# Kernel tuning notes

Hardware: AMD Instinct MI355X
Metric: run time of the kernel (lower is better)

Reference implementation:

```python
import jax, jax.numpy as jnp
import numpy as np

GAMMA = 1.0
MAX_SIMILARITY = 1.0


def setup_inputs() -> dict:
    key = jax.random.key(0)
    k1, k2 = jax.random.split(key)
    B, Ns, D = 128, 512, 256
    d_vectors = jax.random.normal(k1, (B, Ns, D), dtype=jnp.float32)
    # Normalized similarity matrix (MinMaxScaler output lies in [0, 1])
    S = jax.random.uniform(k2, (Ns, Ns), dtype=jnp.float32)
    return {"d_vectors": d_vectors, "S": S}


def reference(d_vectors, S):
    B, Ns, D = d_vectors.shape
    eye = jnp.eye(Ns, dtype=d_vectors.dtype)

    # Pairwise squared distances: ||di||^2 + ||dj||^2 - 2 di.dj  -> [B, Ns, Ns]
    n2 = jnp.sum(d_vectors * d_vectors, axis=-1)  # [B, Ns]
    sq = n2[:, :, None] + n2[:, None, :] - 2.0 * jnp.einsum("bid,bjd->bij", d_vectors, d_vectors)
    sq = jnp.maximum(sq, 0.0) * (1.0 - eye)  # exact zero on the diagonal

    # Safe sqrt (subgradient 0 at zero distance, matching torch.norm)
    dist = jnp.where(sq > 0, jnp.sqrt(jnp.where(sq > 0, sq, 1.0)), 0.0)
    Kd = jnp.exp(-GAMMA * dist)  # Gaussian-kernel Gram matrix [B, Ns, Ns]

    # Norm-ratio loss
    W = (S > 0).astype(d_vectors.dtype)  # [Ns, Ns]
    denom = jnp.linalg.norm(W - eye)  # Frobenius norm, scalar
    Kd_tilde = Kd * (1.0 - eye)  # zero diagonal
    S_tilde = S - MAX_SIMILARITY * eye
    diff = W * (Kd_tilde - S_tilde)  # broadcast over batch
    numer = jnp.sqrt(jnp.sum(diff * diff, axis=(1, 2)))  # [B]
    losses = 2.0 * numer / denom
    return jnp.sum(losses)
```

## Files before the change

kernel.cpp:

```cpp
#include <hip/hip_runtime.h>
#include <hip/hip_bf16.h>

typedef __bf16 bf16_t;
typedef __bf16 bf16x4 __attribute__((ext_vector_type(4)));
typedef __bf16 bf16x8 __attribute__((ext_vector_type(8)));
typedef float f32x4 __attribute__((ext_vector_type(4)));
typedef float f32x16 __attribute__((ext_vector_type(16)));
typedef long i64x2 __attribute__((ext_vector_type(2)));
typedef int i32x4 __attribute__((ext_vector_type(4)));

#define BATCH 128
#define NS 512
#define DIM 256
#define NTB 20
#define LDSP 272
#define CST 68

__global__ __launch_bounds__(256) void prep_st_kernel(const float* __restrict__ dv,
                                                      const float* __restrict__ S,
                                                      unsigned char* __restrict__ f8,
                                                      float* __restrict__ n2g,
                                                      float* __restrict__ St,
                                                      float* __restrict__ dpartial) {
    const int bidx = blockIdx.x;
    const int t = threadIdx.x;
    if (bidx < 256) {
        const int bi = bidx >> 4, bj = bidx & 15;
        const int c  = t & 31, r0 = t >> 5;
        __shared__ float tileS[32][33];
        __shared__ float red[4];
        float dacc = 0.0f;
#pragma unroll
        for (int k = 0; k < 4; ++k) {
            const int r  = r0 + k * 8;
            const int gi = bi * 32 + r, gj = bj * 32 + c;
            const float s = S[(size_t)gi * NS + gj];
            tileS[r][c] = s;
            const float w = (s > 0.0f) ? 1.0f : 0.0f;
            const float e = (gi == gj) ? 1.0f : 0.0f;
            const float d = w - e;
            dacc += d * d;
        }
        __syncthreads();
#pragma unroll
        for (int k = 0; k < 4; ++k) {
            const int r = r0 + k * 8;
            St[(size_t)(bj * 32 + r) * NS + bi * 32 + c] = tileS[c][r];
        }
        const int lane = t & 63, wave = t >> 6;
#pragma unroll
        for (int off = 32; off >= 1; off >>= 1) dacc += __shfl_down(dacc, off, 64);
        if (lane == 0) red[wave] = dacc;
        __syncthreads();
        if (t == 0) dpartial[bidx] = red[0] + red[1] + red[2] + red[3];
    } else {
        const int wid  = ((bidx - 256) << 2) | (t >> 6);
        const int lane = t & 63;
#pragma unroll
        for (int it = 0; it < 8; ++it) {
            const int row = wid + it * 8192;
            const f32x4 v = *reinterpret_cast<const f32x4*>(dv + (size_t)row * DIM + lane * 4);
            float pn = v[0]*v[0] + v[1]*v[1] + v[2]*v[2] + v[3]*v[3];
#pragma unroll
            for (int off = 32; off >= 1; off >>= 1) pn += __shfl_xor(pn, off, 64);
            int w0 = __builtin_amdgcn_cvt_pk_fp8_f32(v[0], v[1], 0, false);
            w0     = __builtin_amdgcn_cvt_pk_fp8_f32(v[2], v[3], w0, true);
            *reinterpret_cast<int*>(f8 + (size_t)row * DIM + lane * 4) = w0;
            if (lane == 0) n2g[row] = pn;
        }
    }
}

__global__ __launch_bounds__(512, 6) void gram_pair_kernel(const unsigned char* __restrict__ f8,
                                                           const float* __restrict__ n2g,
                                                           const float* __restrict__ S,
                                                           const float* __restrict__ St,
                                                           float* __restrict__ partial) {
    const int bid  = blockIdx.x;
    const int work = (bid & 7) * 320 + (bid >> 3);
    const int b    = work / NTB;
    const int r20  = work - b * NTB;
    int ti, tjc;
    if (r20 < 8)       { ti = 0; tjc = r20; }
    else if (r20 < 14) { ti = 1; tjc = r20 - 6; }
    else if (r20 < 18) { ti = 2; tjc = r20 - 10; }
    else               { ti = 3; tjc = r20 - 12; }
    const bool single = ((tjc >> 1) == ti);
    const int t    = threadIdx.x;
    const int wave = t >> 6, lane = t & 63;
    const int wr   = wave >> 1, wc = wave & 1;
    const int col  = lane & 31, kh = lane >> 5;

    __shared__ __attribute__((aligned(16))) char smem[192 * LDSP];
    __shared__ float n2s[192];
    __shared__ float red[8];
    char*  sP = smem;
    float* sC = reinterpret_cast<float*>(smem);

    {
        const unsigned char* srcA = f8 + ((size_t)b * NS + (size_t)ti * 128) * DIM;
#pragma unroll
        for (int it = 0; it < 4; ++it) {
            const i32x4 v = *reinterpret_cast<const i32x4*>(srcA + it * 8192 + t * 16);
            *reinterpret_cast<i32x4*>(&sP[(it * 32 + (t >> 4)) * LDSP + (t & 15) * 16]) = v;
        }
        const unsigned char* srcB = f8 + ((size_t)b * NS + (size_t)tjc * 64) * DIM;
#pragma unroll
        for (int it = 0; it < 2; ++it) {
            const i32x4 v = *reinterpret_cast<const i32x4*>(srcB + it * 8192 + t * 16);
            *reinterpret_cast<i32x4*>(&sP[(128 + it * 32 + (t >> 4)) * LDSP + (t & 15) * 16]) = v;
        }
        if (t < 128)      n2s[t] = n2g[(size_t)b * NS + (size_t)ti * 128 + t];
        else if (t < 192) n2s[t] = n2g[(size_t)b * NS + (size_t)tjc * 64 + (t - 128)];
    }
    __syncthreads();

    const char* aP = &sP[(wr * 32 + col) * LDSP + kh * 16];
    const char* bP = &sP[(128 + wc * 32 + col) * LDSP + kh * 16];
    f32x16 acc = (f32x16)(0.0f);
    __builtin_amdgcn_s_setprio(1);
#pragma unroll
    for (int u = 0; u < 8; ++u) {
        const i64x2 Av = *reinterpret_cast<const i64x2*>(aP + u * 32);
        const i64x2 Bv = *reinterpret_cast<const i64x2*>(bP + u * 32);
        acc = __builtin_amdgcn_mfma_f32_32x32x16_fp8_fp8(Av[0], Bv[0], acc, 0, 0, 0);
        acc = __builtin_amdgcn_mfma_f32_32x32x16_fp8_fp8(Av[1], Bv[1], acc, 0, 0, 0);
    }
    __builtin_amdgcn_s_setprio(0);
    __syncthreads();

    {
        const int lj = wc * 32 + col;
        const float n2j = n2s[128 + lj];
#pragma unroll
        for (int h4 = 0; h4 < 4; ++h4) {
#pragma unroll
            for (int e = 0; e < 4; ++e) {
                const int li = wr * 32 + h4 * 8 + kh * 4 + e;
                const float c = acc[h4 * 4 + e];
                const float sq = fmaxf(n2s[li] + n2j - 2.0f * c, 0.0f);
                sC[li * CST + lj] = __expf(-__builtin_amdgcn_sqrtf(sq));
            }
        }
    }
    __syncthreads();

    float local = 0.0f;
    {
        const int rg = t >> 4;
        const int ln = t & 15;
        f32x4 s1a[4], s2a[4];
#pragma unroll
        for (int p = 0; p < 4; ++p) {
            const int li = p * 32 + rg;
            const int gi = ti * 128 + li;
            const int cb = tjc * 64 + ln * 4;
            s1a[p] = *reinterpret_cast<const f32x4*>(S + (size_t)gi * NS + cb);
            s2a[p] = single ? (f32x4)(0.0f)
                            : *reinterpret_cast<const f32x4*>(St + (size_t)gi * NS + cb);
        }
#pragma unroll
        for (int p = 0; p < 4; ++p) {
            const int li = p * 32 + rg;
            const int gi = ti * 128 + li;
            const f32x4 kdv = *reinterpret_cast<const f32x4*>(&sC[li * CST + ln * 4]);
#pragma unroll
            for (int e = 0; e < 4; ++e) {
                const int gj = tjc * 64 + ln * 4 + e;
                const float kd = kdv[e];
                const float s1 = s1a[p][e];
                if (single) {
                    float d = (gi == gj) ? (1.0f - s1) : (kd - s1);
                    d *= (s1 > 0.0f) ? 1.0f : 0.0f;
                    local += d * d;
                } else {
                    const float s2 = s2a[p][e];
                    const float d1 = (s1 > 0.0f) ? (kd - s1) : 0.0f;
                    const float d2 = (s2 > 0.0f) ? (kd - s2) : 0.0f;
                    local += d1 * d1 + d2 * d2;
                }
            }
        }
    }

#pragma unroll
    for (int off = 32; off >= 1; off >>= 1) local += __shfl_down(local, off, 64);
    if (lane == 0) red[wave] = local;
    __syncthreads();
    if (t == 0) {
        float s = 0.0f;
#pragma unroll
        for (int w = 0; w < 8; ++w) s += red[w];
        partial[(size_t)b * NTB + r20] = s;
    }
}


__global__ __launch_bounds__(256) void norms_kernel(const float* __restrict__ dv,
                                                    float* __restrict__ n2) {
    const int row  = blockIdx.x * 4 + (threadIdx.x >> 6);
    const int lane = threadIdx.x & 63;
    const float4 v = *reinterpret_cast<const float4*>(dv + (size_t)row * DIM + lane * 4);
    float s = v.x * v.x + v.y * v.y + v.z * v.z + v.w * v.w;
#pragma unroll
    for (int off = 32; off >= 1; off >>= 1) s += __shfl_down(s, off, 64);
    if (lane == 0) n2[row] = s;
}

__global__ __launch_bounds__(256) void denom_kernel(const float* __restrict__ Smat,
                                                    float* __restrict__ dpartial) {
    const int t = threadIdx.x;
    const int lane = t & 63, wave = t >> 6;
    __shared__ float sred[4];
    float acc = 0.0f;
    const int base = blockIdx.x * 512;
#pragma unroll
    for (int r = 0; r < 2; ++r) {
        const int v4 = base + r * 256 + t;
        const float4 s4 = reinterpret_cast<const float4*>(Smat)[v4];
        const int idx0 = v4 * 4;
        const int i = idx0 >> 9;
#pragma unroll
        for (int c = 0; c < 4; ++c) {
            const float s = (&s4.x)[c];
            const int j = (idx0 + c) & (NS - 1);
            const float w = (s > 0.0f) ? 1.0f : 0.0f;
            const float e = (i == j) ? 1.0f : 0.0f;
            const float d = w - e;
            acc += d * d;
        }
    }
#pragma unroll
    for (int off = 32; off >= 1; off >>= 1) acc += __shfl_down(acc, off, 64);
    if (lane == 0) sred[wave] = acc;
    __syncthreads();
    if (t == 0) dpartial[blockIdx.x] = sred[0] + sred[1] + sred[2] + sred[3];
}

#define FLDSK 40
__global__ __launch_bounds__(256) void gram_f32_kernel(const float* __restrict__ dv,
                                                       const float* __restrict__ Smat,
                                                       const float* __restrict__ n2,
                                                       float* __restrict__ partial) {
    const int tile = blockIdx.x;
    const int b    = blockIdx.y;
    const int ti   = tile >> 2, tj = tile & 3;
    const int t    = threadIdx.x;
    const int wave = t >> 6, lane = t & 63;
    const int wr   = wave >> 1, wc = wave & 1;

    __shared__ bf16_t sA[128 * FLDSK];
    __shared__ bf16_t sB[128 * FLDSK];
    __shared__ float red[4];

    const float* Abase = dv + ((size_t)b * NS + (size_t)ti * 128) * DIM;
    const float* Bbase = dv + ((size_t)b * NS + (size_t)tj * 128) * DIM;

    f32x4 acc[4][4];
#pragma unroll
    for (int m = 0; m < 4; ++m)
#pragma unroll
        for (int n = 0; n < 4; ++n) acc[m][n] = (f32x4)(0.0f);

    const int fr = lane & 15;
    const int g  = lane >> 4;

    for (int ks = 0; ks < DIM; ks += 32) {
        float4 ra[4], rb[4];
#pragma unroll
        for (int i = 0; i < 4; ++i) {
            const int c   = i * 256 + t;
            const int row = c >> 3;
            const int kc  = (c & 7) * 4;
            ra[i] = *reinterpret_cast<const float4*>(Abase + (size_t)row * DIM + ks + kc);
            rb[i] = *reinterpret_cast<const float4*>(Bbase + (size_t)row * DIM + ks + kc);
        }
        __syncthreads();
#pragma unroll
        for (int i = 0; i < 4; ++i) {
            const int c   = i * 256 + t;
            const int row = c >> 3;
            const int kc  = (c & 7) * 4;
            bf16x4 va = { (bf16_t)ra[i].x, (bf16_t)ra[i].y, (bf16_t)ra[i].z, (bf16_t)ra[i].w };
            bf16x4 vb = { (bf16_t)rb[i].x, (bf16_t)rb[i].y, (bf16_t)rb[i].z, (bf16_t)rb[i].w };
            *reinterpret_cast<bf16x4*>(&sA[row * FLDSK + kc]) = va;
            *reinterpret_cast<bf16x4*>(&sB[row * FLDSK + kc]) = vb;
        }
        __syncthreads();

        bf16x8 afrag[4], bfrag[4];
#pragma unroll
        for (int m = 0; m < 4; ++m)
            afrag[m] = *reinterpret_cast<const bf16x8*>(&sA[(wr * 64 + m * 16 + fr) * FLDSK + g * 8]);
#pragma unroll
        for (int n = 0; n < 4; ++n)
            bfrag[n] = *reinterpret_cast<const bf16x8*>(&sB[(wc * 64 + n * 16 + fr) * FLDSK + g * 8]);
#pragma unroll
        for (int m = 0; m < 4; ++m)
#pragma unroll
            for (int n = 0; n < 4; ++n)
                acc[m][n] = __builtin_amdgcn_mfma_f32_16x16x32_bf16(afrag[m], bfrag[n], acc[m][n], 0, 0, 0);
    }

    float local = 0.0f;
    const float* n2b = n2 + (size_t)b * NS;
    const int rowbase = ti * 128 + wr * 64;
    const int colbase = tj * 128 + wc * 64;
#pragma unroll
    for (int m = 0; m < 4; ++m) {
#pragma unroll
        for (int n = 0; n < 4; ++n) {
            const int gi0 = rowbase + m * 16 + g * 4;
            const int gj  = colbase + n * 16 + fr;
            const float ncol = n2b[gj];
#pragma unroll
            for (int j = 0; j < 4; ++j) {
                const int gi = gi0 + j;
                const float cij = acc[m][n][j];
                float sq = fmaxf(n2b[gi] + ncol - 2.0f * cij, 0.0f);
                const float dist = sqrtf(sq);
                const float kd = __expf(-dist);
                const float s = Smat[(size_t)gi * NS + gj];
                const float w = (s > 0.0f) ? 1.0f : 0.0f;
                float d = (gi == gj) ? (1.0f - s) : (kd - s);
                d *= w;
                local += d * d;
            }
        }
    }
#pragma unroll
    for (int off = 32; off >= 1; off >>= 1) local += __shfl_down(local, off, 64);
    if (lane == 0) red[wave] = local;
    __syncthreads();
    if (t == 0) partial[(size_t)b * 16 + tile] = red[0] + red[1] + red[2] + red[3];
}

__global__ __launch_bounds__(256) void finalize_kernel(const float* __restrict__ dpartial, int ndp,
                                                       const float* __restrict__ partial, int ntiles,
                                                       float* __restrict__ out) {
    const int t = threadIdx.x;
    const int lane = t & 63, wave = t >> 6;
    __shared__ float sred[4];
    __shared__ float sred2[4];

    float dacc = (t < ndp) ? dpartial[t] : 0.0f;
#pragma unroll
    for (int off = 32; off >= 1; off >>= 1) dacc += __shfl_down(dacc, off, 64);
    if (lane == 0) sred[wave] = dacc;
    __syncthreads();
    const float denom = sqrtf(sred[0] + sred[1] + sred[2] + sred[3]);

    float lsum = 0.0f;
    if (t < BATCH) {
        float ss = 0.0f;
        for (int k = 0; k < ntiles; ++k) ss += partial[(size_t)t * ntiles + k];
        lsum = 2.0f * sqrtf(ss) / denom;
    }
#pragma unroll
    for (int off = 32; off >= 1; off >>= 1) lsum += __shfl_down(lsum, off, 64);
    if (lane == 0) sred2[wave] = lsum;
    __syncthreads();
    if (t == 0) out[0] = sred2[0] + sred2[1] + sred2[2] + sred2[3];
}

extern "C" void kernel_launch(void* const* d_in, const int* in_sizes, int n_in,
                              void* d_out, int out_size, void* d_ws, size_t ws_size,
                              hipStream_t stream) {
    const float* dv   = (const float*)d_in[0];
    const float* Smat = (const float*)d_in[1];
    float* out = (float*)d_out;

    const size_t f8_bytes = (size_t)BATCH * NS * DIM;
    const size_t st_bytes = (size_t)NS * NS * 4;
    const size_t n2_bytes = (size_t)BATCH * NS * 4;
    const size_t pt_bytes = (size_t)BATCH * NTB * 4;
    const size_t dp_bytes = 256 * 4;
    const size_t need = f8_bytes + st_bytes + n2_bytes + pt_bytes + dp_bytes;

    if (ws_size >= need) {
        char* w = (char*)d_ws;
        unsigned char* f8 = (unsigned char*)w;  w += f8_bytes;
        float* St      = (float*)w;   w += st_bytes;
        float* n2g     = (float*)w;   w += n2_bytes;
        float* partial = (float*)w;   w += pt_bytes;
        float* dpart   = (float*)w;

        prep_st_kernel<<<dim3(2304), 256, 0, stream>>>(dv, Smat, f8, n2g, St, dpart);
        gram_pair_kernel<<<dim3(NTB * BATCH), 512, 0, stream>>>(f8, n2g, Smat, St, partial);
        finalize_kernel<<<dim3(1), 256, 0, stream>>>(dpart, 256, partial, NTB, out);
    } else {
        float* n2      = (float*)d_ws;
        float* partial = n2 + (size_t)BATCH * NS;
        float* dpart   = partial + (size_t)BATCH * 16;

        norms_kernel<<<dim3(BATCH * NS / 4), 256, 0, stream>>>(dv, n2);
        denom_kernel<<<dim3(128), 256, 0, stream>>>(Smat, dpart);
        gram_f32_kernel<<<dim3(16, BATCH), 256, 0, stream>>>(dv, Smat, n2, partial);
        finalize_kernel<<<dim3(1), 256, 0, stream>>>(dpart, 128, partial, 16, out);
    }
}
```

Baseline: 44.52 us.

## Fuse finalize into gram kernel via last-block atomic counter; prefetch S loads early

Removes the separate single-block finalize launch by having each gram block bump an atomic counter after writing its partial; the last block reduces the denominator partials and per-batch losses and writes the output. The counter is reset in the prep kernel. The S/St tile loads are also hoisted to the top of the gram kernel so their latency overlaps the fp8 tile staging and MFMA work. This adds a threadfence and atomic per block, and the hoisted loads keep more registers live through the matmul.

```diff
diff --git a/kernel.cpp b/kernel.cpp
--- a/kernel.cpp
+++ b/kernel.cpp
@@ -15,15 +15,18 @@
 #define NTB 20
 #define LDSP 272
 #define CST 68
+#define NGRAM (NTB * BATCH)
 
 __global__ __launch_bounds__(256) void prep_st_kernel(const float* __restrict__ dv,
                                                       const float* __restrict__ S,
                                                       unsigned char* __restrict__ f8,
                                                       float* __restrict__ n2g,
                                                       float* __restrict__ St,
-                                                      float* __restrict__ dpartial) {
+                                                      float* __restrict__ dpartial,
+                                                      unsigned int* __restrict__ counter) {
     const int bidx = blockIdx.x;
     const int t = threadIdx.x;
+    if (bidx == 0 && t == 0) *counter = 0;
     if (bidx < 256) {
         const int bi = bidx >> 4, bj = bidx & 15;
         const int c  = t & 31, r0 = t >> 5;
@@ -75,7 +78,10 @@
                                                            const float* __restrict__ n2g,
                                                            const float* __restrict__ S,
                                                            const float* __restrict__ St,
-                                                           float* __restrict__ partial) {
+                                                           const float* __restrict__ dpart,
+                                                           float* __restrict__ partial,
+                                                           unsigned int* __restrict__ counter,
+                                                           float* __restrict__ out) {
     const int bid  = blockIdx.x;
     const int work = (bid & 7) * 320 + (bid >> 3);
     const int b    = work / NTB;
@@ -94,8 +100,21 @@
     __shared__ __attribute__((aligned(16))) char smem[192 * LDSP];
     __shared__ float n2s[192];
     __shared__ float red[8];
+    __shared__ float bc[1];
     char*  sP = smem;
     float* sC = reinterpret_cast<float*>(smem);
+
+    const int rg = t >> 4;
+    const int ln = t & 15;
+    f32x4 s1a[4], s2a[4];
+#pragma unroll
+    for (int p = 0; p < 4; ++p) {
+        const int gi = ti * 128 + p * 32 + rg;
+        const int cb = tjc * 64 + ln * 4;
+        s1a[p] = *reinterpret_cast<const f32x4*>(S + (size_t)gi * NS + cb);
+        s2a[p] = single ? (f32x4)(0.0f)
+                        : *reinterpret_cast<const f32x4*>(St + (size_t)gi * NS + cb);
+    }
 
     {
         const unsigned char* srcA = f8 + ((size_t)b * NS + (size_t)ti * 128) * DIM;
@@ -146,39 +165,25 @@
     __syncthreads();
 
     float local = 0.0f;
-    {
-        const int rg = t >> 4;
-        const int ln = t & 15;
-        f32x4 s1a[4], s2a[4];
-#pragma unroll
-        for (int p = 0; p < 4; ++p) {
-            const int li = p * 32 + rg;
-            const int gi = ti * 128 + li;
-            const int cb = tjc * 64 + ln * 4;
-            s1a[p] = *reinterpret_cast<const f32x4*>(S + (size_t)gi * NS + cb);
-            s2a[p] = single ? (f32x4)(0.0f)
-                            : *reinterpret_cast<const f32x4*>(St + (size_t)gi * NS + cb);
-        }
-#pragma unroll
-        for (int p = 0; p < 4; ++p) {
-            const int li = p * 32 + rg;
-            const int gi = ti * 128 + li;
-            const f32x4 kdv = *reinterpret_cast<const f32x4*>(&sC[li * CST + ln * 4]);
-#pragma unroll
-            for (int e = 0; e < 4; ++e) {
-                const int gj = tjc * 64 + ln * 4 + e;
-                const float kd = kdv[e];
-                const float s1 = s1a[p][e];
-                if (single) {
-                    float d = (gi == gj) ? (1.0f - s1) : (kd - s1);
-                    d *= (s1 > 0.0f) ? 1.0f : 0.0f;
-                    local += d * d;
-                } else {
-                    const float s2 = s2a[p][e];
-                    const float d1 = (s1 > 0.0f) ? (kd - s1) : 0.0f;
-                    const float d2 = (s2 > 0.0f) ? (kd - s2) : 0.0f;
-                    local += d1 * d1 + d2 * d2;
-                }
+#pragma unroll
+    for (int p = 0; p < 4; ++p) {
+        const int li = p * 32 + rg;
+        const int gi = ti * 128 + li;
+        const f32x4 kdv = *reinterpret_cast<const f32x4*>(&sC[li * CST + ln * 4]);
+#pragma unroll
+        for (int e = 0; e < 4; ++e) {
+            const int gj = tjc * 64 + ln * 4 + e;
+            const float kd = kdv[e];
+            const float s1 = s1a[p][e];
+            if (single) {
+                float d = (gi == gj) ? (1.0f - s1) : (kd - s1);
+                d *= (s1 > 0.0f) ? 1.0f : 0.0f;
+                local += d * d;
+            } else {
+                const float s2 = s2a[p][e];
+                const float d1 = (s1 > 0.0f) ? (kd - s1) : 0.0f;
+                const float d2 = (s2 > 0.0f) ? (kd - s2) : 0.0f;
+                local += d1 * d1 + d2 * d2;
             }
         }
     }
@@ -187,11 +192,50 @@
     for (int off = 32; off >= 1; off >>= 1) local += __shfl_down(local, off, 64);
     if (lane == 0) red[wave] = local;
     __syncthreads();
+    bool last = false;
     if (t == 0) {
         float s = 0.0f;
 #pragma unroll
         for (int w = 0; w < 8; ++w) s += red[w];
         partial[(size_t)b * NTB + r20] = s;
+        __threadfence();
+        const unsigned int old = atomicAdd(counter, 1u);
+        last = (old == (unsigned int)(NGRAM - 1));
+        bc[0] = last ? 1.0f : 0.0f;
+    }
+    __syncthreads();
+    if (bc[0] == 0.0f) return;
+
+    __threadfence();
+    float dacc = (t < 256) ? dpart[t] : 0.0f;
+#pragma unroll
+    for (int off = 32; off >= 1; off >>= 1) dacc += __shfl_down(dacc, off, 64);
+    if (lane == 0) red[wave] = dacc;
+    __syncthreads();
+    if (t == 0) {
+        float s = 0.0f;
+#pragma unroll
+        for (int w = 0; w < 8; ++w) s += red[w];
+        bc[0] = sqrtf(s);
+    }
+    __syncthreads();
+    const float denom = bc[0];
+    float lsum = 0.0f;
+    if (t < BATCH) {
+        float ss = 0.0f;
+#pragma unroll
+        for (int k = 0; k < NTB; ++k) ss += partial[(size_t)t * NTB + k];
+        lsum = 2.0f * sqrtf(ss) / denom;
+    }
+#pragma unroll
+    for (int off = 32; off >= 1; off >>= 1) lsum += __shfl_down(lsum, off, 64);
+    if (lane == 0) red[wave] = lsum;
+    __syncthreads();
+    if (t == 0) {
+        float s = 0.0f;
+#pragma unroll
+        for (int w = 0; w < 8; ++w) s += red[w];
+        out[0] = s;
     }
 }
 
@@ -375,7 +419,8 @@
     const size_t n2_bytes = (size_t)BATCH * NS * 4;
     const size_t pt_bytes = (size_t)BATCH * NTB * 4;
     const size_t dp_bytes = 256 * 4;
-    const size_t need = f8_bytes + st_bytes + n2_bytes + pt_bytes + dp_bytes;
+    const size_t ct_bytes = 64;
+    const size_t need = f8_bytes + st_bytes + n2_bytes + pt_bytes + dp_bytes + ct_bytes;
 
     if (ws_size >= need) {
         char* w = (char*)d_ws;
@@ -383,11 +428,11 @@
         float* St      = (float*)w;   w += st_bytes;
         float* n2g     = (float*)w;   w += n2_bytes;
         float* partial = (float*)w;   w += pt_bytes;
-        float* dpart   = (float*)w;
-
-        prep_st_kernel<<<dim3(2304), 256, 0, stream>>>(dv, Smat, f8, n2g, St, dpart);
-        gram_pair_kernel<<<dim3(NTB * BATCH), 512, 0, stream>>>(f8, n2g, Smat, St, partial);
-        finalize_kernel<<<dim3(1), 256, 0, stream>>>(dpart, 256, partial, NTB, out);
+        float* dpart   = (float*)w;   w += dp_bytes;
+        unsigned int* counter = (unsigned int*)w;
+
+        prep_st_kernel<<<dim3(2304), 256, 0, stream>>>(dv, Smat, f8, n2g, St, dpart, counter);
+        gram_pair_kernel<<<dim3(NGRAM), 512, 0, stream>>>(f8, n2g, Smat, St, dpart, partial, counter, out);
     } else {
         float* n2      = (float*)d_ws;
         float* partial = n2 + (size_t)BATCH * NS;
```

Result: slower. 99.74 us (+124.1%).

## Pre-permute S tiles into MFMA accumulator layout to skip LDS staging of kernel values

Applied to the files above, without the earlier changes.

Adds extra blocks to the prep kernel that gather S and its transpose into a per-tile buffer ordered exactly like the MFMA accumulator lanes. The gram kernel can then compute exp(-dist) in registers and combine it with S directly, so it no longer writes the kernel tile to shared memory or needs two barriers and a re-read. The cost is more prep work with strided gathers from S, plus extra workspace (St is still computed but no longer read by the gram kernel).

```diff
diff --git a/kernel.cpp b/kernel.cpp
--- a/kernel.cpp
+++ b/kernel.cpp
@@ -14,14 +14,22 @@
 #define DIM 256
 #define NTB 20
 #define LDSP 272
-#define CST 68
+
+__device__ __forceinline__ void decode_tile(int r20, int& ti, int& tjc) {
+    if (r20 < 8)       { ti = 0; tjc = r20; }
+    else if (r20 < 14) { ti = 1; tjc = r20 - 6; }
+    else if (r20 < 18) { ti = 2; tjc = r20 - 10; }
+    else               { ti = 3; tjc = r20 - 12; }
+}
 
 __global__ __launch_bounds__(256) void prep_st_kernel(const float* __restrict__ dv,
                                                       const float* __restrict__ S,
                                                       unsigned char* __restrict__ f8,
                                                       float* __restrict__ n2g,
                                                       float* __restrict__ St,
-                                                      float* __restrict__ dpartial) {
+                                                      float* __restrict__ dpartial,
+                                                      float* __restrict__ Sp1,
+                                                      float* __restrict__ Sp2) {
     const int bidx = blockIdx.x;
     const int t = threadIdx.x;
     if (bidx < 256) {
@@ -53,7 +61,7 @@
         if (lane == 0) red[wave] = dacc;
         __syncthreads();
         if (t == 0) dpartial[bidx] = red[0] + red[1] + red[2] + red[3];
-    } else {
+    } else if (bidx < 2304) {
         const int wid  = ((bidx - 256) << 2) | (t >> 6);
         const int lane = t & 63;
 #pragma unroll
@@ -68,34 +76,50 @@
             *reinterpret_cast<int*>(f8 + (size_t)row * DIM + lane * 4) = w0;
             if (lane == 0) n2g[row] = pn;
         }
+    } else {
+        const int bid2 = bidx - 2304;
+        const int r20 = bid2 >> 3, w = bid2 & 7;
+        int ti, tjc;
+        decode_tile(r20, ti, tjc);
+        const bool single = ((tjc >> 1) == ti);
+        const int l = t >> 2, h4 = t & 3;
+        const int wr = w >> 1, wc = w & 1;
+        const int col = l & 31, kh = l >> 5;
+        const int lj  = wc * 32 + col;
+        const int gj  = tjc * 64 + lj;
+        const int li0 = wr * 32 + h4 * 8 + kh * 4;
+        const int gi0 = ti * 128 + li0;
+        const size_t base = ((size_t)(r20 * 8 + w) * 64 + l) * 16 + h4 * 4;
+        f32x4 s1v;
+#pragma unroll
+        for (int e = 0; e < 4; ++e) s1v[e] = S[(size_t)(gi0 + e) * NS + gj];
+        f32x4 s2v = (f32x4)(0.0f);
+        if (!single) s2v = *reinterpret_cast<const f32x4*>(S + (size_t)gj * NS + gi0);
+        *reinterpret_cast<f32x4*>(Sp1 + base) = s1v;
+        *reinterpret_cast<f32x4*>(Sp2 + base) = s2v;
     }
 }
 
 __global__ __launch_bounds__(512, 6) void gram_pair_kernel(const unsigned char* __restrict__ f8,
                                                            const float* __restrict__ n2g,
-                                                           const float* __restrict__ S,
-                                                           const float* __restrict__ St,
+                                                           const float* __restrict__ Sp1,
+                                                           const float* __restrict__ Sp2,
                                                            float* __restrict__ partial) {
     const int bid  = blockIdx.x;
     const int work = (bid & 7) * 320 + (bid >> 3);
     const int b    = work / NTB;
     const int r20  = work - b * NTB;
     int ti, tjc;
-    if (r20 < 8)       { ti = 0; tjc = r20; }
-    else if (r20 < 14) { ti = 1; tjc = r20 - 6; }
-    else if (r20 < 18) { ti = 2; tjc = r20 - 10; }
-    else               { ti = 3; tjc = r20 - 12; }
+    decode_tile(r20, ti, tjc);
     const bool single = ((tjc >> 1) == ti);
     const int t    = threadIdx.x;
     const int wave = t >> 6, lane = t & 63;
     const int wr   = wave >> 1, wc = wave & 1;
     const int col  = lane & 31, kh = lane >> 5;
 
-    __shared__ __attribute__((aligned(16))) char smem[192 * LDSP];
+    __shared__ __attribute__((aligned(16))) char sP[192 * LDSP];
     __shared__ float n2s[192];
     __shared__ float red[8];
-    char*  sP = smem;
-    float* sC = reinterpret_cast<float*>(smem);
 
     {
         const unsigned char* srcA = f8 + ((size_t)b * NS + (size_t)ti * 128) * DIM;
@@ -127,54 +151,33 @@
         acc = __builtin_amdgcn_mfma_f32_32x32x16_fp8_fp8(Av[1], Bv[1], acc, 0, 0, 0);
     }
     __builtin_amdgcn_s_setprio(0);
-    __syncthreads();
-
+
+    float local = 0.0f;
     {
         const int lj = wc * 32 + col;
+        const int gj = tjc * 64 + lj;
         const float n2j = n2s[128 + lj];
+        const float* sp1 = Sp1 + ((size_t)(r20 * 8 + wave) * 64 + lane) * 16;
+        const float* sp2 = Sp2 + ((size_t)(r20 * 8 + wave) * 64 + lane) * 16;
 #pragma unroll
         for (int h4 = 0; h4 < 4; ++h4) {
+            const f32x4 s1v = *reinterpret_cast<const f32x4*>(sp1 + h4 * 4);
+            const f32x4 s2v = *reinterpret_cast<const f32x4*>(sp2 + h4 * 4);
 #pragma unroll
             for (int e = 0; e < 4; ++e) {
                 const int li = wr * 32 + h4 * 8 + kh * 4 + e;
                 const float c = acc[h4 * 4 + e];
                 const float sq = fmaxf(n2s[li] + n2j - 2.0f * c, 0.0f);
-                sC[li * CST + lj] = __expf(-__builtin_amdgcn_sqrtf(sq));
-            }
-        }
-    }
-    __syncthreads();
-
-    float local = 0.0f;
-    {
-        const int rg = t >> 4;
-        const int ln = t & 15;
-        f32x4 s1a[4], s2a[4];
-#pragma unroll
-        for (int p = 0; p < 4; ++p) {
-            const int li = p * 32 + rg;
-            const int gi = ti * 128 + li;
-            const int cb = tjc * 64 + ln * 4;
-            s1a[p] = *reinterpret_cast<const f32x4*>(S + (size_t)gi * NS + cb);
-            s2a[p] = single ? (f32x4)(0.0f)
-                            : *reinterpret_cast<const f32x4*>(St + (size_t)gi * NS + cb);
-        }
-#pragma unroll
-        for (int p = 0; p < 4; ++p) {
-            const int li = p * 32 + rg;
-            const int gi = ti * 128 + li;
-            const f32x4 kdv = *reinterpret_cast<const f32x4*>(&sC[li * CST + ln * 4]);
-#pragma unroll
-            for (int e = 0; e < 4; ++e) {
-                const int gj = tjc * 64 + ln * 4 + e;
-                const float kd = kdv[e];
-                const float s1 = s1a[p][e];
+                const float dist = __builtin_amdgcn_sqrtf(sq);
+                const float kd = __expf(-dist);
+                const float s1 = s1v[e];
                 if (single) {
+                    const int gi = ti * 128 + li;
                     float d = (gi == gj) ? (1.0f - s1) : (kd - s1);
                     d *= (s1 > 0.0f) ? 1.0f : 0.0f;
                     local += d * d;
                 } else {
-                    const float s2 = s2a[p][e];
+                    const float s2 = s2v[e];
                     const float d1 = (s1 > 0.0f) ? (kd - s1) : 0.0f;
                     const float d2 = (s2 > 0.0f) ? (kd - s2) : 0.0f;
                     local += d1 * d1 + d2 * d2;
@@ -373,20 +376,23 @@
     const size_t f8_bytes = (size_t)BATCH * NS * DIM;
     const size_t st_bytes = (size_t)NS * NS * 4;
     const size_t n2_bytes = (size_t)BATCH * NS * 4;
+    const size_t sp_bytes = (size_t)NTB * 8 * 64 * 16 * 4;
     const size_t pt_bytes = (size_t)BATCH * NTB * 4;
     const size_t dp_bytes = 256 * 4;
-    const size_t need = f8_bytes + st_bytes + n2_bytes + pt_bytes + dp_bytes;
+    const size_t need = f8_bytes + st_bytes + n2_bytes + 2 * sp_bytes + pt_bytes + dp_bytes;
 
     if (ws_size >= need) {
         char* w = (char*)d_ws;
         unsigned char* f8 = (unsigned char*)w;  w += f8_bytes;
         float* St      = (float*)w;   w += st_bytes;
         float* n2g     = (float*)w;   w += n2_bytes;
+        float* Sp1     = (float*)w;   w += sp_bytes;
+        float* Sp2     = (float*)w;   w += sp_bytes;
         float* partial = (float*)w;   w += pt_bytes;
         float* dpart   = (float*)w;
 
-        prep_st_kernel<<<dim3(2304), 256, 0, stream>>>(dv, Smat, f8, n2g, St, dpart);
-        gram_pair_kernel<<<dim3(NTB * BATCH), 512, 0, stream>>>(f8, n2g, Smat, St, partial);
+        prep_st_kernel<<<dim3(2464), 256, 0, stream>>>(dv, Smat, f8, n2g, St, dpart, Sp1, Sp2);
+        gram_pair_kernel<<<dim3(NTB * BATCH), 512, 0, stream>>>(f8, n2g, Sp1, Sp2, partial);
         finalize_kernel<<<dim3(1), 256, 0, stream>>>(dpart, 256, partial, NTB, out);
     } else {
         float* n2      = (float*)d_ws;
```

New measurement: 50.91 us. 14.4% more time.
